# Kernel tuning notes

Hardware: AMD Instinct MI355X
Metric: run time of the kernel (lower is better)

## Reference

```python
import jax, jax.numpy as jnp
import numpy as np

N = 40000
E = 640000
IN_CH = 256
HEADS = 4
C = 32  # hidden_channels per head
NEG_SLOPE = 0.2  # PyG GATConv default


def setup_inputs() -> dict:
    key = jax.random.key(0)
    k1, k2, k3, k4, k5, k6 = jax.random.split(key, 6)
    x = jax.random.normal(k1, (N, IN_CH), dtype=jnp.float32)
    edge_index = jax.random.randint(k2, (2, E), 0, N, dtype=jnp.int64)
    batch = jnp.zeros((N,), dtype=jnp.int64)
    # GATConv params (glorot-ish scale)
    W = jax.random.normal(k3, (IN_CH, HEADS * C), dtype=jnp.float32) / np.sqrt(IN_CH)
    att_src = jax.random.normal(k4, (HEADS, C), dtype=jnp.float32) / np.sqrt(C)
    att_dst = jax.random.normal(k5, (HEADS, C), dtype=jnp.float32) / np.sqrt(C)
    bias = jnp.zeros((HEADS * C,), dtype=jnp.float32)
    return {"x": x, "edge_index": edge_index, "batch": batch,
            "W": W, "att_src": att_src, "att_dst": att_dst, "bias": bias}


def _gat_forward(x, src, dst, W, att_src, att_dst, bias):
    n = x.shape[0]
    xp = (x @ W).reshape(n, HEADS, C)                      # [N,H,C]
    a_src = jnp.einsum('nhc,hc->nh', xp, att_src)          # [N,H]
    a_dst = jnp.einsum('nhc,hc->nh', xp, att_dst)          # [N,H]
    e = a_src[src] + a_dst[dst]                            # [E',H]
    e = jnp.where(e > 0, e, NEG_SLOPE * e)                 # LeakyReLU
    # segment softmax over edges grouped by destination node
    e_max = jax.ops.segment_max(e, dst, num_segments=n)    # [N,H]
    e_exp = jnp.exp(e - e_max[dst])                        # [E',H]
    e_sum = jax.ops.segment_sum(e_exp, dst, num_segments=n)
    alpha = e_exp / e_sum[dst]                             # [E',H]
    # (attention dropout p=0.6 is identity in eval mode)
    msgs = alpha[:, :, None] * xp[src]                     # [E',H,C]
    out = jax.ops.segment_sum(msgs, dst, num_segments=n)   # [N,H,C]
    out = out.reshape(n, HEADS * C) + bias                 # concat heads
    return jax.nn.relu(out)


def reference(x, edge_index, batch, W, att_src, att_dst, bias):
    n = x.shape[0]
    loops = jnp.arange(n, dtype=edge_index.dtype)
    src = jnp.concatenate([edge_index[0], loops])          # add self-loops (PyG default)
    dst = jnp.concatenate([edge_index[1], loops])
    return _gat_forward(x, src, dst, W, att_src, att_dst, bias)
```

## Files before the change

### kernel.cpp

```cpp
#include <hip/hip_runtime.h>
#include <hip/hip_bf16.h>
#include <stdint.h>

#define IN_CH 256
#define HC    128
#define HEADS 4
#define CPH   32
#define NEG_SLOPE 0.2f

#define NB3    625
#define BCAP3  1408
#define EPB    4096
#define ALD    264
#define GROWS  32

using f32x4  = __attribute__((ext_vector_type(4))) float;
using bf16x8 = __attribute__((ext_vector_type(8))) short;
using f16x8  = __attribute__((ext_vector_type(8))) _Float16;

__global__ __launch_bounds__(256) void k_prep(const float* __restrict__ W,
                                              unsigned short* __restrict__ wpk,
                                              int* __restrict__ bcur) {
    const int t = threadIdx.x, s = blockIdx.x;
    if (s == 0) for (int i = t; i < NB3; i += 256) bcur[i] = 0;
    __shared__ float Wl[32][128];
#pragma unroll
    for (int j = 0; j < 4; ++j) {
        int idx4 = t + j * 256;
        int kk = idx4 >> 5, c4 = (idx4 & 31) * 4;
        *(float4*)(&Wl[kk][c4]) = *(const float4*)(W + (size_t)(s * 32 + kk) * HC + c4);
    }
    __syncthreads();
#pragma unroll
    for (int j = 0; j < 4; ++j) {
        int o = t + j * 256;
        int lane = o & 63, hilo = (o >> 6) & 1, ct = o >> 7;
        const int kk0 = (lane >> 4) * 8;
        const int col = ct * 16 + (lane & 15);
        unsigned short tmp[8];
#pragma unroll
        for (int e = 0; e < 8; ++e) {
            float f = Wl[kk0 + e][col];
            unsigned int u = __float_as_uint(f);
            if (hilo == 0) {
                tmp[e] = (unsigned short)(u >> 16);
            } else {
                float fl = f - __uint_as_float(u & 0xFFFF0000u);
                tmp[e] = (unsigned short)(__float_as_uint(fl) >> 16);
            }
        }
        uint4 ov;
        ov.x = tmp[0] | ((unsigned int)tmp[1] << 16);
        ov.y = tmp[2] | ((unsigned int)tmp[3] << 16);
        ov.z = tmp[4] | ((unsigned int)tmp[5] << 16);
        ov.w = tmp[6] | ((unsigned int)tmp[7] << 16);
        ((uint4*)wpk)[s * 1024 + o] = ov;
    }
}

__global__ __launch_bounds__(256) void k_work(const float* __restrict__ x,
                                              const unsigned short* __restrict__ wpk,
                                              const float* __restrict__ att_src,
                                              const float* __restrict__ att_dst,
                                              unsigned short* __restrict__ xp,
                                              float* __restrict__ asrc,
                                              float* __restrict__ adst,
                                              const int* __restrict__ ei,
                                              int* __restrict__ bcur,
                                              unsigned int* __restrict__ ebuf,
                                              int E, int n, int nbin) {
    __shared__ __align__(16) char smem[2 * GROWS * ALD * 2];

    if (blockIdx.x < (unsigned)nbin) {
        int* hist = (int*)smem;
        int* base = hist + NB3;
        const int t = threadIdx.x;
        const int e0 = blockIdx.x * EPB;
        const int EN = E + n;
        for (int i = t; i < NB3; i += 256) hist[i] = 0;
        __syncthreads();

        unsigned int pk[16];
        int rk[16];
#pragma unroll
        for (int j = 0; j < 16; ++j) {
            int e = e0 + j * 256 + t;
            if (e < EN) {
                int s, d;
                if (e < E) { s = ei[e]; d = ei[E + e]; } else { s = d = e - E; }
                pk[j] = ((unsigned int)d << 16) | (unsigned int)s;
                rk[j] = atomicAdd(&hist[d >> 6], 1);
            } else {
                pk[j] = 0xFFFFFFFFu;
                rk[j] = 0;
            }
        }
        __syncthreads();
        for (int i = t; i < NB3; i += 256) {
            int c = hist[i];
            base[i] = c ? atomicAdd(&bcur[i], c) : 0;
        }
        __syncthreads();
#pragma unroll
        for (int j = 0; j < 16; ++j) {
            if (pk[j] != 0xFFFFFFFFu) {
                int b = pk[j] >> 22;
                int pos = base[b] + rk[j];
                if (pos < BCAP3)
                    ebuf[(size_t)b * BCAP3 + pos] = pk[j];
            }
        }
        return;
    }

    const int bg = blockIdx.x - nbin;
    const int m0 = bg * GROWS;
    if (m0 >= n) return;
    const int tid = threadIdx.x;
    const int wvl = tid >> 6;
    const int l   = tid & 63;
    const int lr  = l & 15;
    const int q   = l >> 4;
    const int kq  = q * 8;

    unsigned short* sa = (unsigned short*)smem;

    {
        const float* xb = x + (size_t)m0 * IN_CH;
#pragma unroll
        for (int j = 0; j < 8; ++j) {
            int c = tid + j * 256;
            int row = c >> 6, k4 = (c & 63) * 4;
            float4 v = *(const float4*)(xb + (size_t)row * IN_CH + k4);
            ushort4 h, lw;
            {
                unsigned int u = __float_as_uint(v.x);
                h.x = (unsigned short)(u >> 16);
                lw.x = (unsigned short)(__float_as_uint(v.x - __uint_as_float(u & 0xFFFF0000u)) >> 16);
                u = __float_as_uint(v.y);
                h.y = (unsigned short)(u >> 16);
                lw.y = (unsigned short)(__float_as_uint(v.y - __uint_as_float(u & 0xFFFF0000u)) >> 16);
                u = __float_as_uint(v.z);
                h.z = (unsigned short)(u >> 16);
                lw.z = (unsigned short)(__float_as_uint(v.z - __uint_as_float(u & 0xFFFF0000u)) >> 16);
                u = __float_as_uint(v.w);
                h.w = (unsigned short)(u >> 16);
                lw.w = (unsigned short)(__float_as_uint(v.w - __uint_as_float(u & 0xFFFF0000u)) >> 16);
            }
            *(ushort4*)(&sa[row * ALD + k4]) = h;
            *(ushort4*)(&sa[(GROWS + row) * ALD + k4]) = lw;
        }
    }
    __syncthreads();

    f32x4 acc00, acc01, acc10, acc11;
    const f32x4 zero = {0.f, 0.f, 0.f, 0.f};
    acc00 = zero; acc01 = zero; acc10 = zero; acc11 = zero;

    const uint4* wb = (const uint4*)wpk + l;
    const int ctb = wvl * 2;

#pragma unroll
    for (int s = 0; s < 8; ++s) {
        uint4 u_h0 = wb[((s * 8 + ctb + 0) * 2 + 0) * 64];
        uint4 u_l0 = wb[((s * 8 + ctb + 0) * 2 + 1) * 64];
        uint4 u_h1 = wb[((s * 8 + ctb + 1) * 2 + 0) * 64];
        uint4 u_l1 = wb[((s * 8 + ctb + 1) * 2 + 1) * 64];
        bf16x8 bh0 = __builtin_bit_cast(bf16x8, u_h0);
        bf16x8 bl0 = __builtin_bit_cast(bf16x8, u_l0);
        bf16x8 bh1 = __builtin_bit_cast(bf16x8, u_h1);
        bf16x8 bl1 = __builtin_bit_cast(bf16x8, u_l1);
        const int ko = s * 32 + kq;
        {
            bf16x8 ah = *(const bf16x8*)(&sa[(size_t)lr * ALD + ko]);
            bf16x8 al = *(const bf16x8*)(&sa[(size_t)(GROWS + lr) * ALD + ko]);
            acc00 = __builtin_amdgcn_mfma_f32_16x16x32_bf16(al, bh0, acc00, 0, 0, 0);
            acc00 = __builtin_amdgcn_mfma_f32_16x16x32_bf16(ah, bl0, acc00, 0, 0, 0);
            acc00 = __builtin_amdgcn_mfma_f32_16x16x32_bf16(ah, bh0, acc00, 0, 0, 0);
            acc01 = __builtin_amdgcn_mfma_f32_16x16x32_bf16(al, bh1, acc01, 0, 0, 0);
            acc01 = __builtin_amdgcn_mfma_f32_16x16x32_bf16(ah, bl1, acc01, 0, 0, 0);
            acc01 = __builtin_amdgcn_mfma_f32_16x16x32_bf16(ah, bh1, acc01, 0, 0, 0);
        }
        {
            bf16x8 ah = *(const bf16x8*)(&sa[(size_t)(16 + lr) * ALD + ko]);
            bf16x8 al = *(const bf16x8*)(&sa[(size_t)(GROWS + 16 + lr) * ALD + ko]);
            acc10 = __builtin_amdgcn_mfma_f32_16x16x32_bf16(al, bh0, acc10, 0, 0, 0);
            acc10 = __builtin_amdgcn_mfma_f32_16x16x32_bf16(ah, bl0, acc10, 0, 0, 0);
            acc10 = __builtin_amdgcn_mfma_f32_16x16x32_bf16(ah, bh0, acc10, 0, 0, 0);
            acc11 = __builtin_amdgcn_mfma_f32_16x16x32_bf16(al, bh1, acc11, 0, 0, 0);
            acc11 = __builtin_amdgcn_mfma_f32_16x16x32_bf16(ah, bl1, acc11, 0, 0, 0);
            acc11 = __builtin_amdgcn_mfma_f32_16x16x32_bf16(ah, bh1, acc11, 0, 0, 0);
        }
    }

    const float as0 = att_src[(ctb + 0) * 16 + lr], as1 = att_src[(ctb + 1) * 16 + lr];
    const float ad0 = att_dst[(ctb + 0) * 16 + lr], ad1 = att_dst[(ctb + 1) * 16 + lr];
#pragma unroll
    for (int rt = 0; rt < 2; ++rt) {
        const f32x4 a0 = rt ? acc10 : acc00;
        const f32x4 a1 = rt ? acc11 : acc01;
#pragma unroll
        for (int r = 0; r < 4; ++r) {
            float s = a0[r] * as0 + a1[r] * as1;
            float d = a0[r] * ad0 + a1[r] * ad1;
            s += __shfl_xor(s, 1, 64); s += __shfl_xor(s, 2, 64);
            s += __shfl_xor(s, 4, 64); s += __shfl_xor(s, 8, 64);
            d += __shfl_xor(d, 1, 64); d += __shfl_xor(d, 2, 64);
            d += __shfl_xor(d, 4, 64); d += __shfl_xor(d, 8, 64);
            if (lr == 0) {
                int row = m0 + rt * 16 + q * 4 + r;
                asrc[(size_t)row * 4 + wvl] = s;
                adst[(size_t)row * 4 + wvl] = d;
            }
        }
    }

#pragma unroll
    for (int rt = 0; rt < 2; ++rt) {
        const f32x4 a0 = rt ? acc10 : acc00;
        const f32x4 a1 = rt ? acc11 : acc01;
#pragma unroll
        for (int r = 0; r < 4; ++r) {
            int row = m0 + rt * 16 + q * 4 + r;
            unsigned short* xr = xp + (size_t)row * HC + wvl * 32 + lr;
            _Float16 h0 = (_Float16)a0[r];
            _Float16 h1 = (_Float16)a1[r];
            xr[0]  = __builtin_bit_cast(unsigned short, h0);
            xr[16] = __builtin_bit_cast(unsigned short, h1);
        }
    }
}

__global__ __launch_bounds__(512) void k_fgat(const int* __restrict__ bcur,
                                              const unsigned int* __restrict__ ebuf,
                                              const float* __restrict__ asrc,
                                              const float* __restrict__ adst,
                                              const unsigned short* __restrict__ xp,
                                              const float* __restrict__ bias,
                                              float* __restrict__ out, int n) {
    __shared__ unsigned short sL[BCAP3];
    __shared__ int lcnt[64];
    __shared__ int loff[65];
    const int b = blockIdx.x, t = threadIdx.x;
    const int m = min(bcur[b], BCAP3);
    const unsigned int* eb = ebuf + (size_t)b * BCAP3;

    unsigned int pk[3];
#pragma unroll
    for (int j = 0; j < 3; ++j) {
        int i = t + j * 512;
        pk[j] = (i < m) ? eb[i] : 0xFFFFFFFFu;
    }
    if (t < 64) lcnt[t] = 0;
    __syncthreads();
    int rk[3];
#pragma unroll
    for (int j = 0; j < 3; ++j)
        if (pk[j] != 0xFFFFFFFFu)
            rk[j] = atomicAdd(&lcnt[(pk[j] >> 16) & 63], 1);
    __syncthreads();
    if (t < 64) {
        int v = lcnt[t];
        int sum = v;
#pragma unroll
        for (int off = 1; off < 64; off <<= 1) {
            int u = __shfl_up(sum, off, 64);
            if (t >= off) sum += u;
        }
        loff[t] = sum - v;
        if (t == 63) loff[64] = sum;
    }
    __syncthreads();
#pragma unroll
    for (int j = 0; j < 3; ++j)
        if (pk[j] != 0xFFFFFFFFu) {
            int ln = (pk[j] >> 16) & 63;
            sL[loff[ln] + rk[j]] = (unsigned short)(pk[j] & 0xFFFFu);
        }
    __syncthreads();

    const int lane = t & 63;
    const int cl = lane & 15;
    const int eg = lane >> 4;
    const int hh = cl >> 2;
    const float4* bp = (const float4*)bias + cl * 2;
    const float4 b0 = bp[0], b1 = bp[1];

#pragma unroll
    for (int i8 = 0; i8 < 8; ++i8) {
        const int ln = (t >> 6) * 8 + i8;
        const int nd = b * 64 + ln;
        if (nd >= n) continue;
        const int s0 = loff[ln], e0 = loff[ln + 1];
        const float ad2 = adst[(size_t)nd * 4 + hh];

        float4 a0 = make_float4(0.f, 0.f, 0.f, 0.f);
        float4 a1 = make_float4(0.f, 0.f, 0.f, 0.f);
        float Z = 0.f;

        int i = s0;
        for (; i + 8 <= e0; i += 8) {
            int sa = sL[i + eg];
            int sb = sL[i + 4 + eg];
            float ta = asrc[(size_t)sa * 4 + hh] + ad2;
            float tb = asrc[(size_t)sb * 4 + hh] + ad2;
            uint4 ua = *(const uint4*)(xp + (size_t)sa * HC + cl * 8);
            uint4 ub = *(const uint4*)(xp + (size_t)sb * HC + cl * 8);
            f16x8 va = __builtin_bit_cast(f16x8, ua);
            f16x8 vb = __builtin_bit_cast(f16x8, ub);
            ta = ta > 0.f ? ta : NEG_SLOPE * ta;
            tb = tb > 0.f ? tb : NEG_SLOPE * tb;
            float pa = __expf(ta);
            float pb = __expf(tb);
            Z += pa + pb;
            a0.x += pa * (float)va[0]; a0.y += pa * (float)va[1];
            a0.z += pa * (float)va[2]; a0.w += pa * (float)va[3];
            a1.x += pa * (float)va[4]; a1.y += pa * (float)va[5];
            a1.z += pa * (float)va[6]; a1.w += pa * (float)va[7];
            a0.x += pb * (float)vb[0]; a0.y += pb * (float)vb[1];
            a0.z += pb * (float)vb[2]; a0.w += pb * (float)vb[3];
            a1.x += pb * (float)vb[4]; a1.y += pb * (float)vb[5];
            a1.z += pb * (float)vb[6]; a1.w += pb * (float)vb[7];
        }
        for (; i < e0; i += 4) {
            if (i + eg < e0) {
                int s = sL[i + eg];
                float tt = asrc[(size_t)s * 4 + hh] + ad2;
                uint4 u = *(const uint4*)(xp + (size_t)s * HC + cl * 8);
                f16x8 v = __builtin_bit_cast(f16x8, u);
                tt = tt > 0.f ? tt : NEG_SLOPE * tt;
                float p = __expf(tt);
                Z += p;
                a0.x += p * (float)v[0]; a0.y += p * (float)v[1];
                a0.z += p * (float)v[2]; a0.w += p * (float)v[3];
                a1.x += p * (float)v[4]; a1.y += p * (float)v[5];
                a1.z += p * (float)v[6]; a1.w += p * (float)v[7];
            }
        }

#pragma unroll
        for (int off = 16; off < 64; off <<= 1) {
            a0.x += __shfl_xor(a0.x, off, 64); a0.y += __shfl_xor(a0.y, off, 64);
            a0.z += __shfl_xor(a0.z, off, 64); a0.w += __shfl_xor(a0.w, off, 64);
            a1.x += __shfl_xor(a1.x, off, 64); a1.y += __shfl_xor(a1.y, off, 64);
            a1.z += __shfl_xor(a1.z, off, 64); a1.w += __shfl_xor(a1.w, off, 64);
            Z += __shfl_xor(Z, off, 64);
        }

        if (eg == 0) {
            const float rZ = 1.0f / Z;
            float4 o0, o1;
            o0.x = fmaxf(a0.x * rZ + b0.x, 0.f); o0.y = fmaxf(a0.y * rZ + b0.y, 0.f);
            o0.z = fmaxf(a0.z * rZ + b0.z, 0.f); o0.w = fmaxf(a0.w * rZ + b0.w, 0.f);
            o1.x = fmaxf(a1.x * rZ + b1.x, 0.f); o1.y = fmaxf(a1.y * rZ + b1.y, 0.f);
            o1.z = fmaxf(a1.z * rZ + b1.z, 0.f); o1.w = fmaxf(a1.w * rZ + b1.w, 0.f);
            float4* op = (float4*)(out + (size_t)nd * HC) + cl * 2;
            op[0] = o0; op[1] = o1;
        }
    }
}

extern "C" void kernel_launch(void* const* d_in, const int* in_sizes, int n_in,
                              void* d_out, int out_size, void* d_ws, size_t ws_size,
                              hipStream_t stream) {
    const float* x       = (const float*)d_in[0];
    const int*   ei      = (const int*)d_in[1];
    const float* W       = (const float*)d_in[3];
    const float* att_src = (const float*)d_in[4];
    const float* att_dst = (const float*)d_in[5];
    const float* bias    = (const float*)d_in[6];
    float* out = (float*)d_out;

    const int n = in_sizes[0] / IN_CH;
    const int E = in_sizes[1] / 2;
    const int EN = E + n;
    const int nbin = (EN + EPB - 1) / EPB;
    const int ngemm = (n + GROWS - 1) / GROWS;
    const int nbkt = (n + 63) / 64;

    unsigned short* xp = (unsigned short*)d_ws;
    float* asrc = (float*)(xp + (size_t)n * HC);
    float* adst = asrc + (size_t)n * HEADS;
    int*   bcur  = (int*)(adst + (size_t)n * HEADS);
    unsigned int* ebuf = (unsigned int*)(bcur + NB3);
    unsigned short* wpk = (unsigned short*)(((uintptr_t)(ebuf + (size_t)NB3 * BCAP3) + 63) & ~(uintptr_t)63);

    k_prep<<<8, 256, 0, stream>>>(W, wpk, bcur);
    k_work<<<nbin + ngemm, 256, 0, stream>>>(x, wpk, att_src, att_dst,
                                             xp, asrc, adst, ei, bcur, ebuf,
                                             E, n, nbin);
    k_fgat<<<nbkt, 512, 0, stream>>>(bcur, ebuf, asrc, adst, xp, bias, out, n);
}
```

Before: 63.70 us.

## Drop low-part split of x in GEMM and unroll edge gather loop by 16

The projection GEMM stops splitting x into high and low bf16 parts. It keeps only the high part, which halves shared memory and removes one of the three MFMAs per tile. The aggregation kernel gains a 16-edge unrolled loop that issues four gathers before consuming them, to give more memory-level parallelism. Truncating x to bf16 with no low-part compensation reduces precision of xp and the attention logits, which may break tolerance.

```diff
diff --git a/kernel.cpp b/kernel.cpp
--- a/kernel.cpp
+++ b/kernel.cpp
@@ -69,7 +69,7 @@
                                               int* __restrict__ bcur,
                                               unsigned int* __restrict__ ebuf,
                                               int E, int n, int nbin) {
-    __shared__ __align__(16) char smem[2 * GROWS * ALD * 2];
+    __shared__ __align__(16) char smem[GROWS * ALD * 2];
 
     if (blockIdx.x < (unsigned)nbin) {
         int* hist = (int*)smem;
@@ -132,23 +132,12 @@
             int c = tid + j * 256;
             int row = c >> 6, k4 = (c & 63) * 4;
             float4 v = *(const float4*)(xb + (size_t)row * IN_CH + k4);
-            ushort4 h, lw;
-            {
-                unsigned int u = __float_as_uint(v.x);
-                h.x = (unsigned short)(u >> 16);
-                lw.x = (unsigned short)(__float_as_uint(v.x - __uint_as_float(u & 0xFFFF0000u)) >> 16);
-                u = __float_as_uint(v.y);
-                h.y = (unsigned short)(u >> 16);
-                lw.y = (unsigned short)(__float_as_uint(v.y - __uint_as_float(u & 0xFFFF0000u)) >> 16);
-                u = __float_as_uint(v.z);
-                h.z = (unsigned short)(u >> 16);
-                lw.z = (unsigned short)(__float_as_uint(v.z - __uint_as_float(u & 0xFFFF0000u)) >> 16);
-                u = __float_as_uint(v.w);
-                h.w = (unsigned short)(u >> 16);
-                lw.w = (unsigned short)(__float_as_uint(v.w - __uint_as_float(u & 0xFFFF0000u)) >> 16);
-            }
+            ushort4 h;
+            h.x = (unsigned short)(__float_as_uint(v.x) >> 16);
+            h.y = (unsigned short)(__float_as_uint(v.y) >> 16);
+            h.z = (unsigned short)(__float_as_uint(v.z) >> 16);
+            h.w = (unsigned short)(__float_as_uint(v.w) >> 16);
             *(ushort4*)(&sa[row * ALD + k4]) = h;
-            *(ushort4*)(&sa[(GROWS + row) * ALD + k4]) = lw;
         }
     }
     __syncthreads();
@@ -173,21 +162,15 @@
         const int ko = s * 32 + kq;
         {
             bf16x8 ah = *(const bf16x8*)(&sa[(size_t)lr * ALD + ko]);
-            bf16x8 al = *(const bf16x8*)(&sa[(size_t)(GROWS + lr) * ALD + ko]);
-            acc00 = __builtin_amdgcn_mfma_f32_16x16x32_bf16(al, bh0, acc00, 0, 0, 0);
             acc00 = __builtin_amdgcn_mfma_f32_16x16x32_bf16(ah, bl0, acc00, 0, 0, 0);
             acc00 = __builtin_amdgcn_mfma_f32_16x16x32_bf16(ah, bh0, acc00, 0, 0, 0);
-            acc01 = __builtin_amdgcn_mfma_f32_16x16x32_bf16(al, bh1, acc01, 0, 0, 0);
             acc01 = __builtin_amdgcn_mfma_f32_16x16x32_bf16(ah, bl1, acc01, 0, 0, 0);
             acc01 = __builtin_amdgcn_mfma_f32_16x16x32_bf16(ah, bh1, acc01, 0, 0, 0);
         }
         {
             bf16x8 ah = *(const bf16x8*)(&sa[(size_t)(16 + lr) * ALD + ko]);
-            bf16x8 al = *(const bf16x8*)(&sa[(size_t)(GROWS + 16 + lr) * ALD + ko]);
-            acc10 = __builtin_amdgcn_mfma_f32_16x16x32_bf16(al, bh0, acc10, 0, 0, 0);
             acc10 = __builtin_amdgcn_mfma_f32_16x16x32_bf16(ah, bl0, acc10, 0, 0, 0);
             acc10 = __builtin_amdgcn_mfma_f32_16x16x32_bf16(ah, bh0, acc10, 0, 0, 0);
-            acc11 = __builtin_amdgcn_mfma_f32_16x16x32_bf16(al, bh1, acc11, 0, 0, 0);
             acc11 = __builtin_amdgcn_mfma_f32_16x16x32_bf16(ah, bl1, acc11, 0, 0, 0);
             acc11 = __builtin_amdgcn_mfma_f32_16x16x32_bf16(ah, bh1, acc11, 0, 0, 0);
         }
@@ -299,6 +282,27 @@
         float Z = 0.f;
 
         int i = s0;
+        for (; i + 16 <= e0; i += 16) {
+            int ss[4]; uint4 uu[4]; float tt[4];
+#pragma unroll
+            for (int j = 0; j < 4; ++j) ss[j] = sL[i + j * 4 + eg];
+#pragma unroll
+            for (int j = 0; j < 4; ++j) uu[j] = *(const uint4*)(xp + (size_t)ss[j] * HC + cl * 8);
+#pragma unroll
+            for (int j = 0; j < 4; ++j) tt[j] = asrc[(size_t)ss[j] * 4 + hh] + ad2;
+#pragma unroll
+            for (int j = 0; j < 4; ++j) {
+                f16x8 v = __builtin_bit_cast(f16x8, uu[j]);
+                float e = tt[j];
+                e = e > 0.f ? e : NEG_SLOPE * e;
+                float p = __expf(e);
+                Z += p;
+                a0.x += p * (float)v[0]; a0.y += p * (float)v[1];
+                a0.z += p * (float)v[2]; a0.w += p * (float)v[3];
+                a1.x += p * (float)v[4]; a1.y += p * (float)v[5];
+                a1.z += p * (float)v[6]; a1.w += p * (float)v[7];
+            }
+        }
         for (; i + 8 <= e0; i += 8) {
             int sa = sL[i + eg];
             int sb = sL[i + 4 + eg];
```

Result: faster. 62.26 us (-2.3%).
